# Performance work log

Measured on AMD Instinct MI355X. Metric: run time of the kernel, lower is better.

Reference implementation:

```python
import jax, jax.numpy as jnp
import numpy as np
from jax.scipy.special import logsumexp

EPS = 0.1
MAX_ITER = 50
THRESH = 1e-9


def _cost_matrix(x, y, p=2):
    # |x_i - y_j|^p summed over feature dim -> (N, P1, P2)
    return jnp.sum(jnp.abs(x[:, :, None, :] - y[:, None, :, :]) ** p, axis=-1)


def _sinkhorn_uv(C, eps, max_iter):
    # Log-domain Sinkhorn iterations; C is treated as a constant (torch no_grad).
    N, P1, P2 = C.shape
    log_mu = jnp.log(jnp.full((N, P1), 1.0 / P1, C.dtype) + 1e-8)
    log_nu = jnp.log(jnp.full((N, P2), 1.0 / P2, C.dtype) + 1e-8)

    def M(u, v):
        return (-C + u[:, :, None] + v[:, None, :]) / eps

    def cond(state):
        u, v, err, it = state
        return jnp.logical_and(it < max_iter, err >= THRESH)

    def body(state):
        u, v, err, it = state
        u1 = u
        u = eps * (log_mu - logsumexp(M(u, v), axis=-1)) + u
        v = eps * (log_nu - logsumexp(M(u, v), axis=-2)) + v
        err = jnp.mean(jnp.sum(jnp.abs(u - u1), axis=-1))
        return (u, v, err, it + 1)

    u0 = jnp.zeros((N, P1), C.dtype)
    v0 = jnp.zeros((N, P2), C.dtype)
    u, v, _, _ = jax.lax.while_loop(cond, body, (u0, v0, jnp.inf, 0))
    return u, v


def setup_inputs() -> dict:
    key = jax.random.key(0)
    kx, ky = jax.random.split(key)
    x = jax.random.normal(kx, (4, 2048, 64), dtype=jnp.float32)
    y = jax.random.normal(ky, (4, 2048, 64), dtype=jnp.float32)
    return {"x": x, "y": y}


def reference(x, y):
    C = _cost_matrix(x, y)
    # u, v computed under no_grad in torch -> constants w.r.t. x, y
    U, V = _sinkhorn_uv(jax.lax.stop_gradient(C), EPS, MAX_ITER)
    pi = jnp.exp((-C + U[:, :, None] + V[:, None, :]) / EPS)
    cost = jnp.sum(pi * C, axis=(-2, -1))  # reduction='none' -> (N,)
    return (cost, pi, C)
```

## Files before the change

### kernel.cpp

```cpp
#include <hip/hip_runtime.h>
#include <math.h>

#define NB 4
#define P 2048
#define DF 64
#define EPS 0.1f
#define INV_EPS 10.0f
#define MAX_ITER 50
#define NBLK 256
#define TPB 512
#define RPB 32
#define NPROD 64
#define SCALE 14.426950408889634f
#define C2N 0.069314718055994531f

typedef float vfloat4 __attribute__((ext_vector_type(4)));

#if __has_builtin(__builtin_amdgcn_exp2f)
#define EXP2(x) __builtin_amdgcn_exp2f(x)
#else
#define EXP2(x) exp2f(x)
#endif
#if __has_builtin(__builtin_amdgcn_logf)
#define LOG2(x) __builtin_amdgcn_logf(x)
#else
#define LOG2(x) log2f(x)
#endif

struct BuildMem { float xs[RPB * DF]; float ys[32 * 260]; };
struct IterMem  { float v[P]; float m[4][P]; float s[4][P]; };
struct RedMem   { float mm[8][32]; float ss[8][32]; };
union SMem { BuildMem b; IterMem c; RedMem r; };

__device__ __forceinline__ void flag_store(unsigned* f, unsigned v) {
  __hip_atomic_store(f, v, __ATOMIC_RELAXED, __HIP_MEMORY_SCOPE_AGENT);
}
__device__ __forceinline__ unsigned flag_load(unsigned* f) {
  return __hip_atomic_load(f, __ATOMIC_RELAXED, __HIP_MEMORY_SCOPE_AGENT);
}
__device__ __forceinline__ float2 load_f2_agent(float2* p) {
  unsigned long long bits = __hip_atomic_load((unsigned long long*)p,
      __ATOMIC_RELAXED, __HIP_MEMORY_SCOPE_AGENT);
  return make_float2(__uint_as_float((unsigned)bits),
                     __uint_as_float((unsigned)(bits >> 32)));
}
__device__ __forceinline__ float load_f_agent(float* p) {
  return __hip_atomic_load(p, __ATOMIC_RELAXED, __HIP_MEMORY_SCOPE_AGENT);
}
__device__ __forceinline__ void store_f_agent(float* p, float v) {
  __hip_atomic_store(p, v, __ATOMIC_RELAXED, __HIP_MEMORY_SCOPE_AGENT);
}

__device__ __forceinline__ void lse_merge(float& M, float& S, float om, float os) {
  float d = EXP2(-fabsf(M - om));
  float Sn = (M >= om) ? fmaf(os, d, S) : fmaf(S, d, os);
  M = fmaxf(M, om);
  S = Sn;
}

__global__ __launch_bounds__(TPB, 2) void sinkhorn_all(
    const float* __restrict__ x, const float* __restrict__ y,
    float* __restrict__ Cout, float* __restrict__ pi,
    float* __restrict__ cost, float* __restrict__ part,
    float* __restrict__ Vg, unsigned* __restrict__ flags, float l2mu) {
  __shared__ SMem sm;
  const int t = threadIdx.x;
  const int w = t >> 6;
  const int l = t & 63;
  const int b = blockIdx.x;
  const int n = b >> 6;
  const int rb = b & 63;
  const int i0 = rb * RPB;
  const size_t xyb = (size_t)n * P * DF;
  const size_t cb = (size_t)n * P * P;
  unsigned* pf = flags + n * NPROD;
  unsigned* vf = flags + 256 + n * NPROD;
  unsigned* ef = flags + 512;
  float* pbase = part + (((size_t)n) << 6) * P;
  float* prow = pbase + (size_t)rb * P;
  float* Vgn = Vg + n * P;

  float creg[4][32];

  {
    const int rr = t >> 4, d4 = (t & 15) * 4;
    float4 xv = *(const float4*)(x + xyb + (size_t)(i0 + rr) * DF + d4);
    sm.b.xs[rr * DF + d4 + 0] = xv.x;
    sm.b.xs[rr * DF + d4 + 1] = xv.y;
    sm.b.xs[rr * DF + d4 + 2] = xv.z;
    sm.b.xs[rr * DF + d4 + 3] = xv.w;
  }
  const int cl = t >> 1;
  const int db = (t & 1) * 16;
#pragma unroll
  for (int k = 0; k < 8; ++k) {
    float acc[4][4];
#pragma unroll
    for (int r = 0; r < 4; ++r) acc[r][0] = acc[r][1] = acc[r][2] = acc[r][3] = 0.f;
#pragma unroll
    for (int h = 0; h < 2; ++h) {
      __syncthreads();
      {
        const float* yp = y + xyb + (size_t)(256 * k + cl) * DF + 32 * h + db;
        float4 q0 = *(const float4*)(yp + 0);
        float4 q1 = *(const float4*)(yp + 4);
        float4 q2 = *(const float4*)(yp + 8);
        float4 q3 = *(const float4*)(yp + 12);
        float* ys = sm.b.ys;
        ys[(db + 0) * 260 + cl] = q0.x;  ys[(db + 1) * 260 + cl] = q0.y;
        ys[(db + 2) * 260 + cl] = q0.z;  ys[(db + 3) * 260 + cl] = q0.w;
        ys[(db + 4) * 260 + cl] = q1.x;  ys[(db + 5) * 260 + cl] = q1.y;
        ys[(db + 6) * 260 + cl] = q1.z;  ys[(db + 7) * 260 + cl] = q1.w;
        ys[(db + 8) * 260 + cl] = q2.x;  ys[(db + 9) * 260 + cl] = q2.y;
        ys[(db + 10) * 260 + cl] = q2.z; ys[(db + 11) * 260 + cl] = q2.w;
        ys[(db + 12) * 260 + cl] = q3.x; ys[(db + 13) * 260 + cl] = q3.y;
        ys[(db + 14) * 260 + cl] = q3.z; ys[(db + 15) * 260 + cl] = q3.w;
      }
      __syncthreads();
#pragma unroll 8
      for (int dd = 0; dd < 32; ++dd) {
        float4 y4 = *(const float4*)&sm.b.ys[dd * 260 + 4 * l];
#pragma unroll
        for (int r = 0; r < 4; ++r) {
          float xv = sm.b.xs[(w * 4 + r) * DF + 32 * h + dd];
          float d0 = xv - y4.x; acc[r][0] = fmaf(d0, d0, acc[r][0]);
          float d1 = xv - y4.y; acc[r][1] = fmaf(d1, d1, acc[r][1]);
          float d2 = xv - y4.z; acc[r][2] = fmaf(d2, d2, acc[r][2]);
          float d3 = xv - y4.w; acc[r][3] = fmaf(d3, d3, acc[r][3]);
        }
      }
    }
#pragma unroll
    for (int r = 0; r < 4; ++r) {
      vfloat4 c4 = {acc[r][0], acc[r][1], acc[r][2], acc[r][3]};
      __builtin_nontemporal_store(c4,
          (vfloat4*)(Cout + cb + (size_t)(i0 + 4 * w + r) * P + 256 * k + 4 * l));
      creg[r][4 * k + 0] = acc[r][0] * SCALE;
      creg[r][4 * k + 1] = acc[r][1] * SCALE;
      creg[r][4 * k + 2] = acc[r][2] * SCALE;
      creg[r][4 * k + 3] = acc[r][3] * SCALE;
    }
  }
  __syncthreads();

  float U[4];
#pragma unroll 1
  for (int it = 0; it < MAX_ITER; ++it) {
    if (t < NPROD) {
      unsigned* f = vf + t;
      while (flag_load(f) < (unsigned)it) __builtin_amdgcn_s_sleep(1);
    }
    __syncthreads();
    {
      float2 a = load_f2_agent((float2*)(Vgn + 4 * t));
      float2 b2 = load_f2_agent((float2*)(Vgn + 4 * t + 2));
      vfloat4 vv = {a.x, a.y, b2.x, b2.y};
      *(vfloat4*)&sm.c.v[4 * t] = vv;
    }
    __syncthreads();
    float vreg[32];
#pragma unroll
    for (int i = 0; i < 32; ++i)
      vreg[i] = sm.c.v[256 * (i >> 2) + 64 * (i & 3) + l];
#pragma unroll
    for (int r = 0; r < 4; ++r) {
      float arg[32];
      float m = -3.4e38f;
#pragma unroll
      for (int i = 0; i < 32; ++i) {
        arg[i] = vreg[i] - creg[r][i];
        m = fmaxf(m, arg[i]);
      }
#pragma unroll
      for (int off = 32; off; off >>= 1) m = fmaxf(m, __shfl_xor(m, off));
      float s = 0.f;
#pragma unroll
      for (int i = 0; i < 32; ++i) s += EXP2(arg[i] - m);
#pragma unroll
      for (int off = 32; off; off >>= 1) s += __shfl_xor(s, off);
      U[r] = l2mu - (m + LOG2(s));
    }
    float pm[32], ps[32];
#pragma unroll
    for (int i = 0; i < 32; ++i) {
      float a0 = U[0] - creg[0][i];
      float a1 = U[1] - creg[1][i];
      float a2 = U[2] - creg[2][i];
      float a3 = U[3] - creg[3][i];
      float m = fmaxf(fmaxf(a0, a1), fmaxf(a2, a3));
      pm[i] = m;
      ps[i] = EXP2(a0 - m) + EXP2(a1 - m) + EXP2(a2 - m) + EXP2(a3 - m);
    }
    if (w >= 4) {
#pragma unroll
      for (int i = 0; i < 32; ++i) {
        int idx = 256 * (i >> 2) + 64 * (i & 3) + l;
        sm.c.m[w - 4][idx] = pm[i];
        sm.c.s[w - 4][idx] = ps[i];
      }
    }
    __syncthreads();
    if (w < 4) {
#pragma unroll
      for (int i = 0; i < 32; ++i) {
        int idx = 256 * (i >> 2) + 64 * (i & 3) + l;
        float M = pm[i], S = ps[i];
        lse_merge(M, S, sm.c.m[w][idx], sm.c.s[w][idx]);
        sm.c.m[w][idx] = M;
        sm.c.s[w][idx] = S;
      }
    }
    __syncthreads();
#pragma unroll
    for (int q = 0; q < 4; ++q) {
      int idx = t + 512 * q;
      float m0 = sm.c.m[0][idx], m1 = sm.c.m[1][idx];
      float m2 = sm.c.m[2][idx], m3 = sm.c.m[3][idx];
      float s0 = sm.c.s[0][idx], s1 = sm.c.s[1][idx];
      float s2 = sm.c.s[2][idx], s3 = sm.c.s[3][idx];
      float M = fmaxf(fmaxf(m0, m1), fmaxf(m2, m3));
      float S = s0 * EXP2(m0 - M) + s1 * EXP2(m1 - M)
              + s2 * EXP2(m2 - M) + s3 * EXP2(m3 - M);
      store_f_agent(prow + idx, M + LOG2(S));
    }
    __threadfence_block();
    __syncthreads();
    if (t == 0) flag_store(&pf[rb], (unsigned)(it + 1));

    if (t < NPROD) {
      unsigned* f = pf + t;
      while (flag_load(f) < (unsigned)(it + 1)) __builtin_amdgcn_s_sleep(1);
    }
    __syncthreads();
    {
      const int cs = t & 31;
      const int p = t >> 5;
      const int s = rb * 32 + cs;
      float L0 = load_f_agent(pbase + (size_t)(p + 0) * P + s);
      float L1 = load_f_agent(pbase + (size_t)(p + 16) * P + s);
      float L2 = load_f_agent(pbase + (size_t)(p + 32) * P + s);
      float L3 = load_f_agent(pbase + (size_t)(p + 48) * P + s);
      float M = fmaxf(fmaxf(L0, L1), fmaxf(L2, L3));
      float S = EXP2(L0 - M) + EXP2(L1 - M) + EXP2(L2 - M) + EXP2(L3 - M);
      float Mo = __shfl_xor(M, 32), So = __shfl_xor(S, 32);
      lse_merge(M, S, Mo, So);
      if (l < 32) { sm.r.mm[w][l] = M; sm.r.ss[w][l] = S; }
    }
    __syncthreads();
    if (t < 32) {
      float Mm = sm.r.mm[0][t], Ss = sm.r.ss[0][t];
#pragma unroll
      for (int w2 = 1; w2 < 8; ++w2)
        lse_merge(Mm, Ss, sm.r.mm[w2][t], sm.r.ss[w2][t]);
      store_f_agent(Vgn + rb * 32 + t, l2mu - (Mm + LOG2(Ss)));
    }
    __threadfence_block();
    __syncthreads();
    if (t == 0) flag_store(&vf[rb], (unsigned)(it + 1));
  }

  if (t < NPROD) {
    unsigned* f = vf + t;
    while (flag_load(f) < (unsigned)MAX_ITER) __builtin_amdgcn_s_sleep(1);
  }
  __syncthreads();
  {
    float2 a = load_f2_agent((float2*)(Vgn + 4 * t));
    float2 b2 = load_f2_agent((float2*)(Vgn + 4 * t + 2));
    vfloat4 vv = {a.x, a.y, b2.x, b2.y};
    *(vfloat4*)&sm.c.v[4 * t] = vv;
  }
  __syncthreads();
  float vreg2[32];
#pragma unroll
  for (int i = 0; i < 32; ++i)
    vreg2[i] = sm.c.v[256 * (i >> 2) + 64 * (i & 3) + l];
  if (t == 0) flag_store(&ef[b], 1u);
  if (t < 256) {
    unsigned* f = &ef[t];
    while (flag_load(f) < 1u) __builtin_amdgcn_s_sleep(1);
  }
  __syncthreads();
  float csum = 0.f;
#pragma unroll
  for (int r = 0; r < 4; ++r) {
    const size_t rowb = cb + (size_t)(i0 + 4 * w + r) * P;
#pragma unroll
    for (int k = 0; k < 8; ++k) {
      vfloat4 p4;
      p4.x = EXP2(U[r] + vreg2[4 * k + 0] - creg[r][4 * k + 0]);
      p4.y = EXP2(U[r] + vreg2[4 * k + 1] - creg[r][4 * k + 1]);
      p4.z = EXP2(U[r] + vreg2[4 * k + 2] - creg[r][4 * k + 2]);
      p4.w = EXP2(U[r] + vreg2[4 * k + 3] - creg[r][4 * k + 3]);
      csum += p4.x * creg[r][4 * k + 0] + p4.y * creg[r][4 * k + 1]
            + p4.z * creg[r][4 * k + 2] + p4.w * creg[r][4 * k + 3];
      __builtin_nontemporal_store(p4, (vfloat4*)(pi + rowb + 256 * k + 4 * l));
    }
  }
  float cs = csum * C2N;
#pragma unroll
  for (int off = 32; off; off >>= 1) cs += __shfl_xor(cs, off);
  if (l == 0) atomicAdd(cost + n, cs);
}

__global__ __launch_bounds__(256) void build_c(const float* __restrict__ x,
                                               const float* __restrict__ y,
                                               float* __restrict__ C,
                                               float* __restrict__ CT) {
  __shared__ float xs[DF][68];
  __shared__ float ys[DF][68];
  const int n = blockIdx.z;
  const int i0 = blockIdx.y * 64, j0 = blockIdx.x * 64;
  const int t = threadIdx.x;
  const int lr = t >> 4, c4 = (t & 15) * 4;
  const size_t xb = (size_t)n * P * DF;
  for (int rr = lr; rr < 64; rr += 16) {
    float4 xv = *(const float4*)(x + xb + (size_t)(i0 + rr) * DF + c4);
    float4 yv = *(const float4*)(y + xb + (size_t)(j0 + rr) * DF + c4);
    xs[c4 + 0][rr] = xv.x; xs[c4 + 1][rr] = xv.y;
    xs[c4 + 2][rr] = xv.z; xs[c4 + 3][rr] = xv.w;
    ys[c4 + 0][rr] = yv.x; ys[c4 + 1][rr] = yv.y;
    ys[c4 + 2][rr] = yv.z; ys[c4 + 3][rr] = yv.w;
  }
  __syncthreads();
  const int ty = t >> 4, tx = t & 15;
  float acc[4][4];
#pragma unroll
  for (int e = 0; e < 4; ++e)
#pragma unroll
    for (int f = 0; f < 4; ++f) acc[e][f] = 0.f;
#pragma unroll 4
  for (int d = 0; d < DF; ++d) {
    float4 a4 = *(const float4*)&xs[d][4 * ty];
    float4 b4 = *(const float4*)&ys[d][4 * tx];
    float av[4] = {a4.x, a4.y, a4.z, a4.w};
    float bv[4] = {b4.x, b4.y, b4.z, b4.w};
#pragma unroll
    for (int e = 0; e < 4; ++e)
#pragma unroll
      for (int f = 0; f < 4; ++f) {
        float df = av[e] - bv[f];
        acc[e][f] = fmaf(df, df, acc[e][f]);
      }
  }
  const size_t cbase = (size_t)n * P * P;
#pragma unroll
  for (int e = 0; e < 4; ++e) {
    float4 v4 = make_float4(acc[e][0], acc[e][1], acc[e][2], acc[e][3]);
    *(float4*)(C + cbase + (size_t)(i0 + 4 * ty + e) * P + (j0 + 4 * tx)) = v4;
  }
#pragma unroll
  for (int f = 0; f < 4; ++f) {
    float4 v4 = make_float4(acc[0][f], acc[1][f], acc[2][f], acc[3][f]);
    *(float4*)(CT + cbase + (size_t)(j0 + 4 * tx + f) * P + (i0 + 4 * ty)) = v4;
  }
}

__global__ __launch_bounds__(256) void lse_pass(const float* __restrict__ M,
                                                const float* __restrict__ wv_,
                                                float* __restrict__ out,
                                                float log_w) {
  __shared__ float red[8];
  const int b = blockIdx.x;
  const int n = b >> 11;
  const int t = threadIdx.x;
  const float4* row = (const float4*)(M + (size_t)b * P);
  const float4* wv = (const float4*)(wv_ + (size_t)n * P);
  float4 c0 = row[t], c1 = row[t + 256];
  float4 w0 = wv[t], w1 = wv[t + 256];
  float a[8];
  a[0] = (w0.x - c0.x) * INV_EPS; a[1] = (w0.y - c0.y) * INV_EPS;
  a[2] = (w0.z - c0.z) * INV_EPS; a[3] = (w0.w - c0.w) * INV_EPS;
  a[4] = (w1.x - c1.x) * INV_EPS; a[5] = (w1.y - c1.y) * INV_EPS;
  a[6] = (w1.z - c1.z) * INV_EPS; a[7] = (w1.w - c1.w) * INV_EPS;
  float mx = a[0];
#pragma unroll
  for (int k = 1; k < 8; ++k) mx = fmaxf(mx, a[k]);
#pragma unroll
  for (int o = 32; o > 0; o >>= 1) mx = fmaxf(mx, __shfl_xor(mx, o));
  if ((t & 63) == 0) red[t >> 6] = mx;
  __syncthreads();
  mx = fmaxf(fmaxf(red[0], red[1]), fmaxf(red[2], red[3]));
  float s = 0.f;
#pragma unroll
  for (int k = 0; k < 8; ++k) s += __expf(a[k] - mx);
#pragma unroll
  for (int o = 32; o > 0; o >>= 1) s += __shfl_xor(s, o);
  if ((t & 63) == 0) red[4 + (t >> 6)] = s;
  __syncthreads();
  if (t == 0) {
    float S = red[4] + red[5] + red[6] + red[7];
    out[b] = EPS * (log_w - (mx + __logf(S)));
  }
}

__global__ __launch_bounds__(256) void final_pass(const float* __restrict__ C,
                                                  const float* __restrict__ u,
                                                  const float* __restrict__ v,
                                                  float* __restrict__ pi,
                                                  float* __restrict__ cost) {
  __shared__ float red[4];
  const int b = blockIdx.x;
  const int n = b >> 11;
  const int t = threadIdx.x;
  const float ui = u[b];
  const float4* row = (const float4*)(C + (size_t)b * P);
  const float4* vv = (const float4*)(v + (size_t)n * P);
  float4* prow = (float4*)(pi + (size_t)b * P);
  float local = 0.f;
#pragma unroll
  for (int h = 0; h < 2; ++h) {
    float4 c = row[t + 256 * h];
    float4 vw = vv[t + 256 * h];
    float4 p;
    p.x = __expf((ui + vw.x - c.x) * INV_EPS);
    p.y = __expf((ui + vw.y - c.y) * INV_EPS);
    p.z = __expf((ui + vw.z - c.z) * INV_EPS);
    p.w = __expf((ui + vw.w - c.w) * INV_EPS);
    prow[t + 256 * h] = p;
    local += p.x * c.x + p.y * c.y + p.z * c.z + p.w * c.w;
  }
#pragma unroll
  for (int o = 32; o > 0; o >>= 1) local += __shfl_xor(local, o);
  if ((t & 63) == 0) red[t >> 6] = local;
  __syncthreads();
  if (t == 0) {
    float S = red[0] + red[1] + red[2] + red[3];
    atomicAdd(cost + n, S);
  }
}

extern "C" void kernel_launch(void* const* d_in, const int* in_sizes, int n_in,
                              void* d_out, int out_size, void* d_ws, size_t ws_size,
                              hipStream_t stream) {
  const float* x = (const float*)d_in[0];
  const float* y = (const float*)d_in[1];
  float* cost = (float*)d_out;
  float* pi = cost + 4;
  float* C = pi + (size_t)NB * P * P;
  float* part = pi;
  float* Vg = pi + (size_t)NB * NPROD * P;
  unsigned* flags = (unsigned*)d_ws;

  (void)hipMemsetAsync(cost, 0, NB * sizeof(float), stream);
  (void)hipMemsetAsync(Vg, 0, NB * P * sizeof(float), stream);
  (void)hipMemsetAsync(flags, 0, 4096, stream);

  float lmu = logf(1.0f / (float)P + 1e-8f);
  float l2mu = log2f(1.0f / (float)P + 1e-8f);

  void* args[] = {(void*)&x, (void*)&y, (void*)&C, (void*)&pi,
                  (void*)&cost, (void*)&part, (void*)&Vg, (void*)&flags,
                  (void*)&l2mu};
  hipError_t err = hipLaunchCooperativeKernel((void*)sinkhorn_all, dim3(NBLK),
                                              dim3(TPB), args, 0, stream);
  if (err != hipSuccess) {
    float* u = (float*)d_ws;
    float* v = u + NB * P;
    (void)hipMemsetAsync(v, 0, NB * P * sizeof(float), stream);
    float* CT = pi;
    build_c<<<dim3(32, 32, 4), 256, 0, stream>>>(x, y, C, CT);
    for (int it = 0; it < MAX_ITER; ++it) {
      lse_pass<<<NB * P, 256, 0, stream>>>(C, v, u, lmu);
      lse_pass<<<NB * P, 256, 0, stream>>>(CT, u, v, lmu);
    }
    final_pass<<<NB * P, 256, 0, stream>>>(C, u, v, pi, cost);
  }
}
```

Measured before the change: 1.036 ms.

## Tile cost matrix as 256x256 blocks with row/column group partial LSE exchange

Each block now owns a 256x256 tile instead of a 32-row strip across all columns. Row and column log-sum-exp partials are exchanged only among the 8 blocks sharing a tile row or tile column, using double-buffered scratch and per-group flags. This replaces the old all-to-all 64-producer partial reduction and the global V broadcast. The aim is to cut cross-block synchronisation traffic and per-iteration global reads, at the cost of two group syncs per iteration and more shuffle work for the column reductions.

```diff
diff --git a/kernel.cpp b/kernel.cpp
--- a/kernel.cpp
+++ b/kernel.cpp
@@ -9,10 +9,10 @@
 #define MAX_ITER 50
 #define NBLK 256
 #define TPB 512
-#define RPB 32
-#define NPROD 64
+#define TS 256
 #define SCALE 14.426950408889634f
 #define C2N 0.069314718055994531f
+#define PARF (NB * 8 * 8 * TS)
 
 typedef float vfloat4 __attribute__((ext_vector_type(4)));
 
@@ -27,10 +27,9 @@
 #define LOG2(x) log2f(x)
 #endif
 
-struct BuildMem { float xs[RPB * DF]; float ys[32 * 260]; };
-struct IterMem  { float v[P]; float m[4][P]; float s[4][P]; };
-struct RedMem   { float mm[8][32]; float ss[8][32]; };
-union SMem { BuildMem b; IterMem c; RedMem r; };
+struct BuildMem { float xs[32 * 260]; float ys[32 * 260]; };
+struct IterMem  { float rin[8 * 260]; float red[260]; float cw[8 * 260]; };
+union SMem { BuildMem b; IterMem c; };
 
 __device__ __forceinline__ void flag_store(unsigned* f, unsigned v) {
   __hip_atomic_store(f, v, __ATOMIC_RELAXED, __HIP_MEMORY_SCOPE_AGENT);
@@ -38,14 +37,17 @@
 __device__ __forceinline__ unsigned flag_load(unsigned* f) {
   return __hip_atomic_load(f, __ATOMIC_RELAXED, __HIP_MEMORY_SCOPE_AGENT);
 }
-__device__ __forceinline__ float2 load_f2_agent(float2* p) {
+__device__ __forceinline__ void store_f2_agent(float* p, float a, float b) {
+  unsigned long long bits =
+      ((unsigned long long)__float_as_uint(b) << 32) | __float_as_uint(a);
+  __hip_atomic_store((unsigned long long*)p, bits, __ATOMIC_RELAXED,
+                     __HIP_MEMORY_SCOPE_AGENT);
+}
+__device__ __forceinline__ float2 load_f2_agent(const float* p) {
   unsigned long long bits = __hip_atomic_load((unsigned long long*)p,
       __ATOMIC_RELAXED, __HIP_MEMORY_SCOPE_AGENT);
   return make_float2(__uint_as_float((unsigned)bits),
                      __uint_as_float((unsigned)(bits >> 32)));
-}
-__device__ __forceinline__ float load_f_agent(float* p) {
-  return __hip_atomic_load(p, __ATOMIC_RELAXED, __HIP_MEMORY_SCOPE_AGENT);
 }
 __device__ __forceinline__ void store_f_agent(float* p, float v) {
   __hip_atomic_store(p, v, __ATOMIC_RELAXED, __HIP_MEMORY_SCOPE_AGENT);
@@ -61,107 +63,112 @@
 __global__ __launch_bounds__(TPB, 2) void sinkhorn_all(
     const float* __restrict__ x, const float* __restrict__ y,
     float* __restrict__ Cout, float* __restrict__ pi,
-    float* __restrict__ cost, float* __restrict__ part,
-    float* __restrict__ Vg, unsigned* __restrict__ flags, float l2mu) {
+    float* __restrict__ cost, float* __restrict__ rp,
+    float* __restrict__ cp, unsigned* __restrict__ flags, float l2mu) {
   __shared__ SMem sm;
   const int t = threadIdx.x;
   const int w = t >> 6;
   const int l = t & 63;
+  const int gg = l >> 3;
+  const int c8 = l & 7;
   const int b = blockIdx.x;
   const int n = b >> 6;
-  const int rb = b & 63;
-  const int i0 = rb * RPB;
+  const int bi = (b >> 3) & 7;
+  const int bj = b & 7;
   const size_t xyb = (size_t)n * P * DF;
   const size_t cb = (size_t)n * P * P;
-  unsigned* pf = flags + n * NPROD;
-  unsigned* vf = flags + 256 + n * NPROD;
+  const int r0 = 32 * w + 4 * gg;
+  unsigned* rowflag = flags + (n * 8 + bi) * 8;
+  unsigned* colflag = flags + 256 + (n * 8 + bj) * 8;
   unsigned* ef = flags + 512;
-  float* pbase = part + (((size_t)n) << 6) * P;
-  float* prow = pbase + (size_t)rb * P;
-  float* Vgn = Vg + n * P;
 
   float creg[4][32];
 
-  {
-    const int rr = t >> 4, d4 = (t & 15) * 4;
-    float4 xv = *(const float4*)(x + xyb + (size_t)(i0 + rr) * DF + d4);
-    sm.b.xs[rr * DF + d4 + 0] = xv.x;
-    sm.b.xs[rr * DF + d4 + 1] = xv.y;
-    sm.b.xs[rr * DF + d4 + 2] = xv.z;
-    sm.b.xs[rr * DF + d4 + 3] = xv.w;
-  }
+#pragma unroll
+  for (int r = 0; r < 4; ++r)
+#pragma unroll
+    for (int i = 0; i < 32; ++i) creg[r][i] = 0.f;
+
   const int cl = t >> 1;
   const int db = (t & 1) * 16;
 #pragma unroll
-  for (int k = 0; k < 8; ++k) {
-    float acc[4][4];
-#pragma unroll
-    for (int r = 0; r < 4; ++r) acc[r][0] = acc[r][1] = acc[r][2] = acc[r][3] = 0.f;
-#pragma unroll
-    for (int h = 0; h < 2; ++h) {
-      __syncthreads();
-      {
-        const float* yp = y + xyb + (size_t)(256 * k + cl) * DF + 32 * h + db;
-        float4 q0 = *(const float4*)(yp + 0);
-        float4 q1 = *(const float4*)(yp + 4);
-        float4 q2 = *(const float4*)(yp + 8);
-        float4 q3 = *(const float4*)(yp + 12);
-        float* ys = sm.b.ys;
-        ys[(db + 0) * 260 + cl] = q0.x;  ys[(db + 1) * 260 + cl] = q0.y;
-        ys[(db + 2) * 260 + cl] = q0.z;  ys[(db + 3) * 260 + cl] = q0.w;
-        ys[(db + 4) * 260 + cl] = q1.x;  ys[(db + 5) * 260 + cl] = q1.y;
-        ys[(db + 6) * 260 + cl] = q1.z;  ys[(db + 7) * 260 + cl] = q1.w;
-        ys[(db + 8) * 260 + cl] = q2.x;  ys[(db + 9) * 260 + cl] = q2.y;
-        ys[(db + 10) * 260 + cl] = q2.z; ys[(db + 11) * 260 + cl] = q2.w;
-        ys[(db + 12) * 260 + cl] = q3.x; ys[(db + 13) * 260 + cl] = q3.y;
-        ys[(db + 14) * 260 + cl] = q3.z; ys[(db + 15) * 260 + cl] = q3.w;
+  for (int h = 0; h < 2; ++h) {
+    __syncthreads();
+    {
+      const float* xp = x + xyb + (size_t)(TS * bi + cl) * DF + 32 * h + db;
+      float4 q0 = *(const float4*)(xp + 0);
+      float4 q1 = *(const float4*)(xp + 4);
+      float4 q2 = *(const float4*)(xp + 8);
+      float4 q3 = *(const float4*)(xp + 12);
+      float* xs = sm.b.xs;
+      xs[(db + 0) * 260 + cl] = q0.x;  xs[(db + 1) * 260 + cl] = q0.y;
+      xs[(db + 2) * 260 + cl] = q0.z;  xs[(db + 3) * 260 + cl] = q0.w;
+      xs[(db + 4) * 260 + cl] = q1.x;  xs[(db + 5) * 260 + cl] = q1.y;
+      xs[(db + 6) * 260 + cl] = q1.z;  xs[(db + 7) * 260 + cl] = q1.w;
+      xs[(db + 8) * 260 + cl] = q2.x;  xs[(db + 9) * 260 + cl] = q2.y;
+      xs[(db + 10) * 260 + cl] = q2.z; xs[(db + 11) * 260 + cl] = q2.w;
+      xs[(db + 12) * 260 + cl] = q3.x; xs[(db + 13) * 260 + cl] = q3.y;
+      xs[(db + 14) * 260 + cl] = q3.z; xs[(db + 15) * 260 + cl] = q3.w;
+      const float* yp = y + xyb + (size_t)(TS * bj + cl) * DF + 32 * h + db;
+      q0 = *(const float4*)(yp + 0);
+      q1 = *(const float4*)(yp + 4);
+      q2 = *(const float4*)(yp + 8);
+      q3 = *(const float4*)(yp + 12);
+      float* ys = sm.b.ys;
+      ys[(db + 0) * 260 + cl] = q0.x;  ys[(db + 1) * 260 + cl] = q0.y;
+      ys[(db + 2) * 260 + cl] = q0.z;  ys[(db + 3) * 260 + cl] = q0.w;
+      ys[(db + 4) * 260 + cl] = q1.x;  ys[(db + 5) * 260 + cl] = q1.y;
+      ys[(db + 6) * 260 + cl] = q1.z;  ys[(db + 7) * 260 + cl] = q1.w;
+      ys[(db + 8) * 260 + cl] = q2.x;  ys[(db + 9) * 260 + cl] = q2.y;
+      ys[(db + 10) * 260 + cl] = q2.z; ys[(db + 11) * 260 + cl] = q2.w;
+      ys[(db + 12) * 260 + cl] = q3.x; ys[(db + 13) * 260 + cl] = q3.y;
+      ys[(db + 14) * 260 + cl] = q3.z; ys[(db + 15) * 260 + cl] = q3.w;
+    }
+    __syncthreads();
+#pragma unroll 4
+    for (int dd = 0; dd < 32; ++dd) {
+      float4 x4 = *(const float4*)&sm.b.xs[dd * 260 + r0];
+      float xv[4] = {x4.x, x4.y, x4.z, x4.w};
+#pragma unroll
+      for (int cc = 0; cc < 8; ++cc) {
+        float4 y4 = *(const float4*)&sm.b.ys[dd * 260 + 32 * cc + 4 * c8];
+        float yv[4] = {y4.x, y4.y, y4.z, y4.w};
+#pragma unroll
+        for (int r = 0; r < 4; ++r)
+#pragma unroll
+          for (int e = 0; e < 4; ++e) {
+            float dfv = xv[r] - yv[e];
+            creg[r][4 * cc + e] = fmaf(dfv, dfv, creg[r][4 * cc + e]);
+          }
       }
-      __syncthreads();
-#pragma unroll 8
-      for (int dd = 0; dd < 32; ++dd) {
-        float4 y4 = *(const float4*)&sm.b.ys[dd * 260 + 4 * l];
-#pragma unroll
-        for (int r = 0; r < 4; ++r) {
-          float xv = sm.b.xs[(w * 4 + r) * DF + 32 * h + dd];
-          float d0 = xv - y4.x; acc[r][0] = fmaf(d0, d0, acc[r][0]);
-          float d1 = xv - y4.y; acc[r][1] = fmaf(d1, d1, acc[r][1]);
-          float d2 = xv - y4.z; acc[r][2] = fmaf(d2, d2, acc[r][2]);
-          float d3 = xv - y4.w; acc[r][3] = fmaf(d3, d3, acc[r][3]);
-        }
-      }
-    }
-#pragma unroll
-    for (int r = 0; r < 4; ++r) {
-      vfloat4 c4 = {acc[r][0], acc[r][1], acc[r][2], acc[r][3]};
-      __builtin_nontemporal_store(c4,
-          (vfloat4*)(Cout + cb + (size_t)(i0 + 4 * w + r) * P + 256 * k + 4 * l));
-      creg[r][4 * k + 0] = acc[r][0] * SCALE;
-      creg[r][4 * k + 1] = acc[r][1] * SCALE;
-      creg[r][4 * k + 2] = acc[r][2] * SCALE;
-      creg[r][4 * k + 3] = acc[r][3] * SCALE;
+    }
+  }
+#pragma unroll
+  for (int r = 0; r < 4; ++r) {
+    const size_t rowb = cb + (size_t)(TS * bi + r0 + r) * P + TS * bj;
+#pragma unroll
+    for (int cc = 0; cc < 8; ++cc) {
+      vfloat4 c4 = {creg[r][4 * cc + 0], creg[r][4 * cc + 1],
+                    creg[r][4 * cc + 2], creg[r][4 * cc + 3]};
+      __builtin_nontemporal_store(c4, (vfloat4*)(Cout + rowb + 32 * cc + 4 * c8));
+      creg[r][4 * cc + 0] *= SCALE;
+      creg[r][4 * cc + 1] *= SCALE;
+      creg[r][4 * cc + 2] *= SCALE;
+      creg[r][4 * cc + 3] *= SCALE;
     }
   }
   __syncthreads();
 
   float U[4];
+  float vreg[32];
+#pragma unroll
+  for (int i = 0; i < 32; ++i) vreg[i] = 0.f;
+
 #pragma unroll 1
   for (int it = 0; it < MAX_ITER; ++it) {
-    if (t < NPROD) {
-      unsigned* f = vf + t;
-      while (flag_load(f) < (unsigned)it) __builtin_amdgcn_s_sleep(1);
-    }
-    __syncthreads();
-    {
-      float2 a = load_f2_agent((float2*)(Vgn + 4 * t));
-      float2 b2 = load_f2_agent((float2*)(Vgn + 4 * t + 2));
-      vfloat4 vv = {a.x, a.y, b2.x, b2.y};
-      *(vfloat4*)&sm.c.v[4 * t] = vv;
-    }
-    __syncthreads();
-    float vreg[32];
-#pragma unroll
-    for (int i = 0; i < 32; ++i)
-      vreg[i] = sm.c.v[256 * (i >> 2) + 64 * (i & 3) + l];
+    float* rpp = rp + (it & 1) * PARF;
+    float* cpp = cp + (it & 1) * PARF;
+    float Lrow[4];
 #pragma unroll
     for (int r = 0; r < 4; ++r) {
       float arg[32];
@@ -171,16 +178,51 @@
         arg[i] = vreg[i] - creg[r][i];
         m = fmaxf(m, arg[i]);
       }
-#pragma unroll
-      for (int off = 32; off; off >>= 1) m = fmaxf(m, __shfl_xor(m, off));
+      m = fmaxf(m, __shfl_xor(m, 1));
+      m = fmaxf(m, __shfl_xor(m, 2));
+      m = fmaxf(m, __shfl_xor(m, 4));
       float s = 0.f;
 #pragma unroll
       for (int i = 0; i < 32; ++i) s += EXP2(arg[i] - m);
-#pragma unroll
-      for (int off = 32; off; off >>= 1) s += __shfl_xor(s, off);
-      U[r] = l2mu - (m + LOG2(s));
-    }
-    float pm[32], ps[32];
+      s += __shfl_xor(s, 1);
+      s += __shfl_xor(s, 2);
+      s += __shfl_xor(s, 4);
+      Lrow[r] = m + LOG2(s);
+    }
+    if (c8 == 0) {
+      float* dst = rpp + ((n * 8 + bi) * 8 + bj) * TS + r0;
+      store_f2_agent(dst, Lrow[0], Lrow[1]);
+      store_f2_agent(dst + 2, Lrow[2], Lrow[3]);
+    }
+    __threadfence_block();
+    __syncthreads();
+    if (t == 0) flag_store(&rowflag[bj], (unsigned)(it + 1));
+    if (t < 8) {
+      while (flag_load(&rowflag[t]) < (unsigned)(it + 1)) __builtin_amdgcn_s_sleep(1);
+    }
+    __syncthreads();
+    {
+      const float* src = rpp + (n * 8 + bi) * 8 * TS + 4 * t;
+      float2 a = load_f2_agent(src);
+      float2 b2 = load_f2_agent(src + 2);
+      vfloat4 vv = {a.x, a.y, b2.x, b2.y};
+      *(vfloat4*)&sm.c.rin[(t >> 6) * 260 + (t & 63) * 4] = vv;
+    }
+    __syncthreads();
+    if (t < TS) {
+      float m = sm.c.rin[t];
+#pragma unroll
+      for (int p = 1; p < 8; ++p) m = fmaxf(m, sm.c.rin[p * 260 + t]);
+      float s = 0.f;
+#pragma unroll
+      for (int p = 0; p < 8; ++p) s += EXP2(sm.c.rin[p * 260 + t] - m);
+      sm.c.red[t] = l2mu - (m + LOG2(s));
+    }
+    __syncthreads();
+#pragma unroll
+    for (int r = 0; r < 4; ++r) U[r] = sm.c.red[r0 + r];
+
+    float cm[32], cs_[32];
 #pragma unroll
     for (int i = 0; i < 32; ++i) {
       float a0 = U[0] - creg[0][i];
@@ -188,113 +230,83 @@
       float a2 = U[2] - creg[2][i];
       float a3 = U[3] - creg[3][i];
       float m = fmaxf(fmaxf(a0, a1), fmaxf(a2, a3));
-      pm[i] = m;
-      ps[i] = EXP2(a0 - m) + EXP2(a1 - m) + EXP2(a2 - m) + EXP2(a3 - m);
-    }
-    if (w >= 4) {
+      cm[i] = m;
+      cs_[i] = EXP2(a0 - m) + EXP2(a1 - m) + EXP2(a2 - m) + EXP2(a3 - m);
+    }
+#pragma unroll
+    for (int step = 8; step <= 32; step <<= 1) {
 #pragma unroll
       for (int i = 0; i < 32; ++i) {
-        int idx = 256 * (i >> 2) + 64 * (i & 3) + l;
-        sm.c.m[w - 4][idx] = pm[i];
-        sm.c.s[w - 4][idx] = ps[i];
+        float mo = __shfl_xor(cm[i], step);
+        float so = __shfl_xor(cs_[i], step);
+        lse_merge(cm[i], cs_[i], mo, so);
       }
     }
-    __syncthreads();
-    if (w < 4) {
-#pragma unroll
-      for (int i = 0; i < 32; ++i) {
-        int idx = 256 * (i >> 2) + 64 * (i & 3) + l;
-        float M = pm[i], S = ps[i];
-        lse_merge(M, S, sm.c.m[w][idx], sm.c.s[w][idx]);
-        sm.c.m[w][idx] = M;
-        sm.c.s[w][idx] = S;
-      }
-    }
-    __syncthreads();
-#pragma unroll
-    for (int q = 0; q < 4; ++q) {
-      int idx = t + 512 * q;
-      float m0 = sm.c.m[0][idx], m1 = sm.c.m[1][idx];
-      float m2 = sm.c.m[2][idx], m3 = sm.c.m[3][idx];
-      float s0 = sm.c.s[0][idx], s1 = sm.c.s[1][idx];
-      float s2 = sm.c.s[2][idx], s3 = sm.c.s[3][idx];
-      float M = fmaxf(fmaxf(m0, m1), fmaxf(m2, m3));
-      float S = s0 * EXP2(m0 - M) + s1 * EXP2(m1 - M)
-              + s2 * EXP2(m2 - M) + s3 * EXP2(m3 - M);
-      store_f_agent(prow + idx, M + LOG2(S));
+    if (gg == 0) {
+#pragma unroll
+      for (int i = 0; i < 32; ++i)
+        sm.c.cw[w * 260 + 32 * (i >> 2) + 4 * c8 + (i & 3)] = cm[i] + LOG2(cs_[i]);
+    }
+    __syncthreads();
+    if (t < TS) {
+      float m = sm.c.cw[t];
+#pragma unroll
+      for (int wv = 1; wv < 8; ++wv) m = fmaxf(m, sm.c.cw[wv * 260 + t]);
+      float s = 0.f;
+#pragma unroll
+      for (int wv = 0; wv < 8; ++wv) s += EXP2(sm.c.cw[wv * 260 + t] - m);
+      store_f_agent(cpp + ((n * 8 + bj) * 8 + bi) * TS + t, m + LOG2(s));
     }
     __threadfence_block();
     __syncthreads();
-    if (t == 0) flag_store(&pf[rb], (unsigned)(it + 1));
-
-    if (t < NPROD) {
-      unsigned* f = pf + t;
-      while (flag_load(f) < (unsigned)(it + 1)) __builtin_amdgcn_s_sleep(1);
+    if (t == 0) flag_store(&colflag[bi], (unsigned)(it + 1));
+    if (t < 8) {
+      while (flag_load(&colflag[t]) < (unsigned)(it + 1)) __builtin_amdgcn_s_sleep(1);
     }
     __syncthreads();
     {
-      const int cs = t & 31;
-      const int p = t >> 5;
-      const int s = rb * 32 + cs;
-      float L0 = load_f_agent(pbase + (size_t)(p + 0) * P + s);
-      float L1 = load_f_agent(pbase + (size_t)(p + 16) * P + s);
-      float L2 = load_f_agent(pbase + (size_t)(p + 32) * P + s);
-      float L3 = load_f_agent(pbase + (size_t)(p + 48) * P + s);
-      float M = fmaxf(fmaxf(L0, L1), fmaxf(L2, L3));
-      float S = EXP2(L0 - M) + EXP2(L1 - M) + EXP2(L2 - M) + EXP2(L3 - M);
-      float Mo = __shfl_xor(M, 32), So = __shfl_xor(S, 32);
-      lse_merge(M, S, Mo, So);
-      if (l < 32) { sm.r.mm[w][l] = M; sm.r.ss[w][l] = S; }
-    }
-    __syncthreads();
-    if (t < 32) {
-      float Mm = sm.r.mm[0][t], Ss = sm.r.ss[0][t];
-#pragma unroll
-      for (int w2 = 1; w2 < 8; ++w2)
-        lse_merge(Mm, Ss, sm.r.mm[w2][t], sm.r.ss[w2][t]);
-      store_f_agent(Vgn + rb * 32 + t, l2mu - (Mm + LOG2(Ss)));
-    }
-    __threadfence_block();
-    __syncthreads();
-    if (t == 0) flag_store(&vf[rb], (unsigned)(it + 1));
-  }
-
-  if (t < NPROD) {
-    unsigned* f = vf + t;
-    while (flag_load(f) < (unsigned)MAX_ITER) __builtin_amdgcn_s_sleep(1);
-  }
-  __syncthreads();
-  {
-    float2 a = load_f2_agent((float2*)(Vgn + 4 * t));
-    float2 b2 = load_f2_agent((float2*)(Vgn + 4 * t + 2));
-    vfloat4 vv = {a.x, a.y, b2.x, b2.y};
-    *(vfloat4*)&sm.c.v[4 * t] = vv;
-  }
-  __syncthreads();
-  float vreg2[32];
-#pragma unroll
-  for (int i = 0; i < 32; ++i)
-    vreg2[i] = sm.c.v[256 * (i >> 2) + 64 * (i & 3) + l];
+      const float* src = cpp + (n * 8 + bj) * 8 * TS + 4 * t;
+      float2 a = load_f2_agent(src);
+      float2 b2 = load_f2_agent(src + 2);
+      vfloat4 vv = {a.x, a.y, b2.x, b2.y};
+      *(vfloat4*)&sm.c.rin[(t >> 6) * 260 + (t & 63) * 4] = vv;
+    }
+    __syncthreads();
+    if (t < TS) {
+      float m = sm.c.rin[t];
+#pragma unroll
+      for (int p = 1; p < 8; ++p) m = fmaxf(m, sm.c.rin[p * 260 + t]);
+      float s = 0.f;
+#pragma unroll
+      for (int p = 0; p < 8; ++p) s += EXP2(sm.c.rin[p * 260 + t] - m);
+      sm.c.red[t] = l2mu - (m + LOG2(s));
+    }
+    __syncthreads();
+#pragma unroll
+    for (int i = 0; i < 32; ++i)
+      vreg[i] = sm.c.red[32 * (i >> 2) + 4 * c8 + (i & 3)];
+    __syncthreads();
+  }
+
   if (t == 0) flag_store(&ef[b], 1u);
   if (t < 256) {
-    unsigned* f = &ef[t];
-    while (flag_load(f) < 1u) __builtin_amdgcn_s_sleep(1);
+    while (flag_load(&ef[t]) < 1u) __builtin_amdgcn_s_sleep(1);
   }
   __syncthreads();
   float csum = 0.f;
 #pragma unroll
   for (int r = 0; r < 4; ++r) {
-    const size_t rowb = cb + (size_t)(i0 + 4 * w + r) * P;
-#pragma unroll
-    for (int k = 0; k < 8; ++k) {
+    const size_t rowb = cb + (size_t)(TS * bi + r0 + r) * P + TS * bj;
+#pragma unroll
+    for (int cc = 0; cc < 8; ++cc) {
       vfloat4 p4;
-      p4.x = EXP2(U[r] + vreg2[4 * k + 0] - creg[r][4 * k + 0]);
-      p4.y = EXP2(U[r] + vreg2[4 * k + 1] - creg[r][4 * k + 1]);
-      p4.z = EXP2(U[r] + vreg2[4 * k + 2] - creg[r][4 * k + 2]);
-      p4.w = EXP2(U[r] + vreg2[4 * k + 3] - creg[r][4 * k + 3]);
-      csum += p4.x * creg[r][4 * k + 0] + p4.y * creg[r][4 * k + 1]
-            + p4.z * creg[r][4 * k + 2] + p4.w * creg[r][4 * k + 3];
-      __builtin_nontemporal_store(p4, (vfloat4*)(pi + rowb + 256 * k + 4 * l));
+      p4.x = EXP2(U[r] + vreg[4 * cc + 0] - creg[r][4 * cc + 0]);
+      p4.y = EXP2(U[r] + vreg[4 * cc + 1] - creg[r][4 * cc + 1]);
+      p4.z = EXP2(U[r] + vreg[4 * cc + 2] - creg[r][4 * cc + 2]);
+      p4.w = EXP2(U[r] + vreg[4 * cc + 3] - creg[r][4 * cc + 3]);
+      csum += p4.x * creg[r][4 * cc + 0] + p4.y * creg[r][4 * cc + 1]
+            + p4.z * creg[r][4 * cc + 2] + p4.w * creg[r][4 * cc + 3];
+      __builtin_nontemporal_store(p4, (vfloat4*)(pi + rowb + 32 * cc + 4 * c8));
     }
   }
   float cs = csum * C2N;
@@ -438,19 +450,18 @@
   float* cost = (float*)d_out;
   float* pi = cost + 4;
   float* C = pi + (size_t)NB * P * P;
-  float* part = pi;
-  float* Vg = pi + (size_t)NB * NPROD * P;
+  float* rp = pi;
+  float* cp = pi + 2 * PARF;
   unsigned* flags = (unsigned*)d_ws;
 
   (void)hipMemsetAsync(cost, 0, NB * sizeof(float), stream);
-  (void)hipMemsetAsync(Vg, 0, NB * P * sizeof(float), stream);
   (void)hipMemsetAsync(flags, 0, 4096, stream);
 
   float lmu = logf(1.0f / (float)P + 1e-8f);
   float l2mu = log2f(1.0f / (float)P + 1e-8f);
 
   void* args[] = {(void*)&x, (void*)&y, (void*)&C, (void*)&pi,
-                  (void*)&cost, (void*)&part, (void*)&Vg, (void*)&flags,
+                  (void*)&cost, (void*)&rp, (void*)&cp, (void*)&flags,
                   (void*)&l2mu};
   hipError_t err = hipLaunchCooperativeKernel((void*)sinkhorn_all, dim3(NBLK),
                                               dim3(TPB), args, 0, stream);
```

Result: slower. 1.154 ms (+11.5%).
